# Performance work log

Hardware: AMD Instinct MI355X
Metric: run time of the kernel (lower is better)

The kernel has to match this reference:

```python
import jax, jax.numpy as jnp
import numpy as np

B, S, D = 4, 2048, 768
H, R = 12, 8
Dh = D // H


def setup_inputs() -> dict:
    key = jax.random.key(0)
    ks = jax.random.split(key, 12)
    s_in = 1.0 / np.sqrt(D)
    s_r = 1.0 / np.sqrt(R)
    return {
        "x": jax.random.normal(ks[0], (B, S, D), jnp.float32),
        "Wq0": jax.random.normal(ks[1], (D, D), jnp.float32) * s_in,
        "Aq": jax.random.normal(ks[2], (D, R), jnp.float32) * s_in,
        "Bq": jax.random.normal(ks[3], (R, D), jnp.float32) * s_r,
        "Wk0": jax.random.normal(ks[4], (D, D), jnp.float32) * s_in,
        "Ak": jax.random.normal(ks[5], (D, R), jnp.float32) * s_in,
        "Bk": jax.random.normal(ks[6], (R, D), jnp.float32) * s_r,
        "Wv0": jax.random.normal(ks[7], (D, D), jnp.float32) * s_in,
        "Av": jax.random.normal(ks[8], (D, R), jnp.float32) * s_in,
        "Bv": jax.random.normal(ks[9], (R, D), jnp.float32) * s_r,
        "Wo": jax.random.normal(ks[10], (D, D), jnp.float32) * s_in,
        "bo": jnp.zeros((D,), jnp.float32),
    }


def _lora(x, W0, A, Bm):
    # x @ W0 + (x @ A) @ B  -- low-rank adapter on frozen W0
    return x @ W0 + (x @ A) @ Bm


def _split_heads(t):
    # [B,S,D] -> [B,H,S,Dh]
    return t.reshape(B, S, H, Dh).transpose(0, 2, 1, 3)


def reference(x, Wq0, Aq, Bq, Wk0, Ak, Bk, Wv0, Av, Bv, Wo, bo):
    q = _split_heads(_lora(x, Wq0, Aq, Bq))
    k = _split_heads(_lora(x, Wk0, Ak, Bk))
    v = _split_heads(_lora(x, Wv0, Av, Bv))
    scale = 1.0 / jnp.sqrt(jnp.asarray(Dh, x.dtype))
    scores = jnp.einsum("bhqd,bhkd->bhqk", q, k) * scale  # [B,H,S,S]
    weights = jax.nn.softmax(scores, axis=-1)
    attn = jnp.einsum("bhqk,bhkd->bhqd", weights, v)
    concat = attn.transpose(0, 2, 1, 3).reshape(B, S, D)
    return concat @ Wo + bo
```

## Files before the change

kernel.cpp:

```cpp
#include <hip/hip_runtime.h>
#include <hip/hip_bf16.h>


typedef unsigned short ushort_t;
typedef __bf16 bf16x8 __attribute__((ext_vector_type(8)));
typedef float f32x4 __attribute__((ext_vector_type(4)));
typedef float f32x16 __attribute__((ext_vector_type(16)));
typedef unsigned short ushort8 __attribute__((ext_vector_type(8)));
typedef unsigned short ushort4_t __attribute__((ext_vector_type(4)));
typedef unsigned int uint4v __attribute__((ext_vector_type(4)));
typedef __attribute__((address_space(1))) unsigned int gu32;
typedef __attribute__((address_space(3))) unsigned int lu32;

__device__ __forceinline__ unsigned short f2bf(float f) {
  unsigned int u = __builtin_bit_cast(unsigned int, f);
  u += 0x7fffu + ((u >> 16) & 1u);
  return (unsigned short)(u >> 16);
}

__device__ __forceinline__ void gld_lds16(const void* g, void* s) {
  __builtin_amdgcn_global_load_lds((gu32*)(unsigned long long)g,
                                   (lu32*)(unsigned int)(unsigned long long)s,
                                   16, 0, 0);
}

__device__ __forceinline__ void gld_lds4(const void* g, void* s) {
  __builtin_amdgcn_global_load_lds((gu32*)(unsigned long long)g,
                                   (lu32*)(unsigned int)(unsigned long long)s,
                                   4, 0, 0);
}

__device__ __forceinline__ f32x4 mfma16(bf16x8 a, bf16x8 b, f32x4 c) {
  return __builtin_amdgcn_mfma_f32_16x16x32_bf16(a, b, c, 0, 0, 0);
}

__device__ __forceinline__ f32x16 mfma32(bf16x8 a, bf16x8 b, f32x16 c) {
  return __builtin_amdgcn_mfma_f32_32x32x16_bf16(a, b, c, 0, 0, 0);
}

__device__ __forceinline__ unsigned int cvtpk(float a, float b) {
  unsigned int r;
  asm("v_cvt_pk_bf16_f32 %0, %1, %2" : "=v"(r) : "v"(a), "v"(b));
  return r;
}

__global__ __launch_bounds__(256) void prep_weights(
    const float* __restrict__ Wq0, const float* __restrict__ Aq, const float* __restrict__ Bq,
    const float* __restrict__ Wk0, const float* __restrict__ Ak, const float* __restrict__ Bk,
    const float* __restrict__ Wv0, const float* __restrict__ Av, const float* __restrict__ Bv,
    const float* __restrict__ Wo,
    ushort_t* __restrict__ WeffT, ushort_t* __restrict__ WoT)
{
  __shared__ float tile[32][33];
  __shared__ float tA[32][8];
  __shared__ float tB[8][32];
  const int mat = blockIdx.y;
  const int kt = blockIdx.x / 24, nt = blockIdx.x % 24;
  const int k0 = kt * 32, n0 = nt * 32;
  const float* W0 = (mat == 0) ? Wq0 : (mat == 1) ? Wk0 : (mat == 2) ? Wv0 : Wo;
  const float* Am = (mat == 0) ? Aq : (mat == 1) ? Ak : (mat == 2) ? Av : nullptr;
  const float* Bm = (mat == 0) ? Bq : (mat == 1) ? Bk : (mat == 2) ? Bv : nullptr;
  const int tid = threadIdx.x;
#pragma unroll
  for (int i = 0; i < 4; i++) {
    int rr = i * 8 + (tid >> 5), c = tid & 31;
    tile[rr][c] = W0[(k0 + rr) * 768 + n0 + c];
  }
  if (Am) {
    tA[tid >> 3][tid & 7] = Am[(k0 + (tid >> 3)) * 8 + (tid & 7)];
    tB[tid >> 5][tid & 31] = Bm[(tid >> 5) * 768 + n0 + (tid & 31)];
  }
  __syncthreads();
#pragma unroll
  for (int i = 0; i < 4; i++) {
    int kk = tid & 31;
    int nn = i * 8 + (tid >> 5);
    float val = tile[kk][nn];
    if (Am) {
#pragma unroll
      for (int rr = 0; rr < 8; rr++) val += tA[kk][rr] * tB[rr][nn];
    }
    int n = n0 + nn, kg = k0 + kk;
    if (mat < 3) WeffT[((long)mat * 768 + n) * 768 + kg] = f2bf(val);
    else         WoT[(long)n * 768 + kg] = f2bf(val);
  }
}

__global__ __launch_bounds__(256) void cast_x(const float* __restrict__ x,
                                              ushort_t* __restrict__ xb)
{
  long i = (long)blockIdx.x * 256 + threadIdx.x;
  const float4* xp = (const float4*)x;
  float4 a = xp[i * 2], c = xp[i * 2 + 1];
  ushort8 rv;
  rv[0] = f2bf(a.x); rv[1] = f2bf(a.y); rv[2] = f2bf(a.z); rv[3] = f2bf(a.w);
  rv[4] = f2bf(c.x); rv[5] = f2bf(c.y); rv[6] = f2bf(c.z); rv[7] = f2bf(c.w);
  *(ushort8*)&xb[i * 8] = rv;
}

template <int MODE>
__global__ __launch_bounds__(256) void gemm_bt(
    const ushort_t* __restrict__ A, const ushort_t* __restrict__ Bt,
    ushort_t* __restrict__ q, ushort_t* __restrict__ kbuf, ushort_t* __restrict__ vt,
    float* __restrict__ out, const float* __restrict__ bo)
{
  constexpr int K = 768;
  __shared__ ushort_t As[128 * 64];
  __shared__ ushort_t Bs[128 * 64];
  const int tid = threadIdx.x;
  const int l = tid & 63, w = tid >> 6;
  const int wm = w >> 1, wn = w & 1;
  const int lr = l & 15, lg = l >> 4;
  const long rowBase = (long)blockIdx.x * 128;
  const long colBase = (long)blockIdx.y * 128;
  f32x4 acc[4][4] = {};

  for (int k0 = 0; k0 < K; k0 += 64) {
    __syncthreads();
#pragma unroll
    for (int i = 0; i < 4; i++) {
      int ci = i * 256 + tid;
      gld_lds16(A + (rowBase + (ci >> 3)) * K + k0 + (ci & 7) * 8, &As[ci * 8]);
    }
#pragma unroll
    for (int i = 0; i < 4; i++) {
      int ci = i * 256 + tid;
      gld_lds16(Bt + (colBase + (ci >> 3)) * K + k0 + (ci & 7) * 8, &Bs[ci * 8]);
    }
    asm volatile("s_waitcnt vmcnt(0)" ::: "memory");
    __syncthreads();
#pragma unroll
    for (int ks = 0; ks < 2; ks++) {
      bf16x8 af[4], bf[4];
#pragma unroll
      for (int m = 0; m < 4; m++)
        af[m] = *(const bf16x8*)&As[(wm * 64 + m * 16 + lr) * 64 + ks * 32 + lg * 8];
#pragma unroll
      for (int n = 0; n < 4; n++)
        bf[n] = *(const bf16x8*)&Bs[(wn * 64 + n * 16 + lr) * 64 + ks * 32 + lg * 8];
#pragma unroll
      for (int m = 0; m < 4; m++)
#pragma unroll
        for (int n = 0; n < 4; n++)
          acc[m][n] = mfma16(af[m], bf[n], acc[m][n]);
    }
  }

  if (MODE == 0) {
    const int mat = (int)(colBase / 768);
    if (mat == 2) {
      const long cb = colBase - 1536;
#pragma unroll
      for (int m = 0; m < 4; m++) {
        long srow = rowBase + wm * 64 + m * 16 + lg * 4;
        long b = srow >> 11, s = srow & 2047;
#pragma unroll
        for (int n = 0; n < 4; n++) {
          long col = cb + wn * 64 + n * 16 + lr;
          ushort4_t pk;
#pragma unroll
          for (int r = 0; r < 4; r++) pk[r] = f2bf(acc[m][n][r]);
          *(ushort4_t*)&vt[(b * 768 + col) * 2048 + s] = pk;
        }
      }
    } else {
      ushort_t* dst = (mat == 0) ? q : kbuf;
      const float scl = (mat == 0) ? 0.125f * 1.4426950408889634f : 1.0f;
      const long cb = colBase - (long)mat * 768;
#pragma unroll
      for (int m = 0; m < 4; m++)
#pragma unroll
        for (int n = 0; n < 4; n++) {
          long col = cb + wn * 64 + n * 16 + lr;
#pragma unroll
          for (int r = 0; r < 4; r++) {
            long row = rowBase + wm * 64 + m * 16 + lg * 4 + r;
            dst[row * 768 + col] = f2bf(acc[m][n][r] * scl);
          }
        }
    }
  } else {
#pragma unroll
    for (int m = 0; m < 4; m++)
#pragma unroll
      for (int n = 0; n < 4; n++) {
        long col = colBase + wn * 64 + n * 16 + lr;
        float bv = bo[col];
#pragma unroll
        for (int r = 0; r < 4; r++) {
          long row = rowBase + wm * 64 + m * 16 + lg * 4 + r;
          out[row * 768 + col] = acc[m][n][r] + bv;
        }
      }
  }
}

__global__ __launch_bounds__(256) void attn_fwd(
    const ushort_t* __restrict__ Q, const ushort_t* __restrict__ Kg,
    const ushort_t* __restrict__ VtG, ushort_t* __restrict__ O)
{
  constexpr int D = 768, S = 2048;
  __shared__ ushort_t Ks[2][64 * 64];
  __shared__ ushort_t Vs[2][64 * 64];
  const int tid = threadIdx.x;
  const int l = tid & 63, w = tid >> 6;
  const int q32 = l & 31, hi = l >> 5;
  const int i = blockIdx.x;
  const int xcd = i & 7, j = i >> 3;
  const int bh = xcd * 6 + (j >> 4);
  const int q0 = (j & 15) * 128;
  const int b = bh / 12, h = bh % 12;
  const ushort_t* Qb = Q + (long)b * S * D + h * 64;
  const ushort_t* Kb = Kg + (long)b * S * D + h * 64;
  const ushort_t* Vb = VtG + ((long)b * 768 + h * 64) * S;

  bf16x8 qf[4];
  {
    const ushort_t* qrow = Qb + (long)(q0 + w * 32 + q32) * D + hi * 8;
#pragma unroll
    for (int ks = 0; ks < 4; ks++) qf[ks] = *(const bf16x8*)&qrow[ks * 16];
  }

  int koff[2];
#pragma unroll
  for (int it = 0; it < 2; it++) {
    int ci = it * 256 + tid, r = ci >> 3, bp = ci & 7;
    koff[it] = r * D + ((bp ^ (r & 7)) * 8);
  }
  int voff[8];
#pragma unroll
  for (int it = 0; it < 8; it++) {
    int vi = it * 256 + tid;
    int d = vi >> 5, c_l = (vi >> 2) & 7, slot = vi & 3;
    int c = c_l ^ (d & 7);
    int p = c * 8 + slot * 2;
    int a = p >> 4, hp = (p >> 3) & 1, jj = p & 7;
    int key = 32 * (a >> 1) + 16 * (a & 1) + 8 * (jj >> 2) + (jj & 3) + 4 * hp;
    voff[it] = d * S + key;
  }

  bf16x8 ones;
#pragma unroll
  for (int e = 0; e < 8; e++) ones[e] = (__bf16)1.0f;

  f32x16 oA = {}, oB = {}, osum = {};
  const int swz = q32 & 7;

  auto STAGE = [&](int kt, int bi) {
    const ushort_t* kp = Kb + (long)kt * 64 * D;
#pragma unroll
    for (int it = 0; it < 2; it++)
      gld_lds16(kp + koff[it], &Ks[bi][(it * 256 + tid) * 8]);
    const ushort_t* vp = Vb + kt * 64;
#pragma unroll
    for (int it = 0; it < 8; it++)
      gld_lds4(vp + voff[it], &Vs[bi][(it * 256 + tid) * 2]);
  };

  STAGE(0, 0);

  for (int kt = 0; kt < 32; kt++) {
    const int cur = kt & 1;
    STAGE((kt + 1) & 31, cur ^ 1);
    asm volatile("s_waitcnt vmcnt(10)" ::: "memory");
    __builtin_amdgcn_s_barrier();

    const ushort_t* ksb = &Ks[cur][0];
    const ushort_t* vsb = &Vs[cur][0];

    f32x16 s0 = {}, s1 = {};
    __builtin_amdgcn_s_setprio(1);
#pragma unroll
    for (int ks = 0; ks < 4; ks++) {
      int ch = ((ks * 2 + hi) ^ swz) * 8;
      bf16x8 kf0 = *(const bf16x8*)&ksb[q32 * 64 + ch];
      bf16x8 kf1 = *(const bf16x8*)&ksb[(32 + q32) * 64 + ch];
      s0 = mfma32(kf0, qf[ks], s0);
      s1 = mfma32(kf1, qf[ks], s1);
    }
    __builtin_amdgcn_s_setprio(0);

    unsigned int pw[16];
#pragma unroll
    for (int u = 0; u < 8; u++) {
      float a0 = __builtin_amdgcn_exp2f(s0[2 * u]);
      float a1 = __builtin_amdgcn_exp2f(s0[2 * u + 1]);
      pw[u] = cvtpk(a0, a1);
    }
#pragma unroll
    for (int u = 0; u < 8; u++) {
      float a0 = __builtin_amdgcn_exp2f(s1[2 * u]);
      float a1 = __builtin_amdgcn_exp2f(s1[2 * u + 1]);
      pw[8 + u] = cvtpk(a0, a1);
    }

    __builtin_amdgcn_s_setprio(1);
#pragma unroll
    for (int ks = 0; ks < 4; ks++) {
      uint4v w4 = {pw[4 * ks], pw[4 * ks + 1], pw[4 * ks + 2], pw[4 * ks + 3]};
      bf16x8 pa = __builtin_bit_cast(bf16x8, w4);
      int ch = ((ks * 2 + hi) ^ swz) * 8;
      bf16x8 vf0 = *(const bf16x8*)&vsb[q32 * 64 + ch];
      bf16x8 vf1 = *(const bf16x8*)&vsb[(32 + q32) * 64 + ch];
      oA = mfma32(pa, vf0, oA);
      oB = mfma32(pa, vf1, oB);
      osum = mfma32(pa, ones, osum);
    }
    __builtin_amdgcn_s_setprio(0);

    asm volatile("" ::: "memory");
    __builtin_amdgcn_s_barrier();
  }

#pragma unroll
  for (int reg = 0; reg < 16; reg++) {
    int row = (reg & 3) + 8 * (reg >> 2) + 4 * hi;
    float inv = 1.0f / osum[reg];
    long base = ((long)b * S + q0 + w * 32 + row) * D + h * 64 + q32;
    O[base] = f2bf(oA[reg] * inv);
    O[base + 32] = f2bf(oB[reg] * inv);
  }
}

extern "C" void kernel_launch(void* const* d_in, const int* in_sizes, int n_in,
                              void* d_out, int out_size, void* d_ws, size_t ws_size,
                              hipStream_t stream)
{
  const float* x   = (const float*)d_in[0];
  const float* Wq0 = (const float*)d_in[1];
  const float* Aq  = (const float*)d_in[2];
  const float* Bq  = (const float*)d_in[3];
  const float* Wk0 = (const float*)d_in[4];
  const float* Ak  = (const float*)d_in[5];
  const float* Bk  = (const float*)d_in[6];
  const float* Wv0 = (const float*)d_in[7];
  const float* Av  = (const float*)d_in[8];
  const float* Bv  = (const float*)d_in[9];
  const float* Wo  = (const float*)d_in[10];
  const float* bo  = (const float*)d_in[11];
  float* out = (float*)d_out;

  char* ws = (char*)d_ws;
  const long SZ = 8192L * 768 * 2;
  ushort_t* xb    = (ushort_t*)(ws);
  ushort_t* Qb    = (ushort_t*)(ws + SZ);
  ushort_t* Kb    = (ushort_t*)(ws + 2 * SZ);
  ushort_t* Vt    = (ushort_t*)(ws + 3 * SZ);
  ushort_t* At    = (ushort_t*)(ws + 4 * SZ);
  ushort_t* WeffT = (ushort_t*)(ws + 5 * SZ);
  ushort_t* WoT   = (ushort_t*)(ws + 5 * SZ + 2304L * 768 * 2);

  hipLaunchKernelGGL(prep_weights, dim3(576, 4), dim3(256), 0, stream,
                     Wq0, Aq, Bq, Wk0, Ak, Bk, Wv0, Av, Bv, Wo, WeffT, WoT);
  hipLaunchKernelGGL(cast_x, dim3(3072), dim3(256), 0, stream, x, xb);
  hipLaunchKernelGGL((gemm_bt<0>), dim3(64, 18), dim3(256), 0, stream,
                     xb, WeffT, Qb, Kb, Vt, (float*)nullptr, (const float*)nullptr);
  hipLaunchKernelGGL(attn_fwd, dim3(768), dim3(256), 0, stream, Qb, Kb, Vt, At);
  hipLaunchKernelGGL((gemm_bt<1>), dim3(64, 6), dim3(256), 0, stream,
                     At, WoT, (ushort_t*)nullptr, (ushort_t*)nullptr, (ushort_t*)nullptr,
                     out, bo);
}
```

Measured before the change: 174.9 us.

## Pre-permute V^T key order in projection epilogue to enable 16-byte LDS loads

The V-projection epilogue now writes V^T with key positions permuted (bits 2 and 3 of the sequence index swapped), matching the order the P-fragment MFMA layout expects. The attention kernel can then stage V tiles with two 16-byte global-to-LDS loads per thread instead of eight 4-byte loads, using the same XOR swizzle as K. The wait count is lowered to match, and the per-ks read offsets are precomputed. This couples the producer layout to the consumer's register layout, so any mismatch would silently give wrong results.

```diff
diff --git a/kernel.cpp b/kernel.cpp
--- a/kernel.cpp
+++ b/kernel.cpp
@@ -22,12 +22,6 @@
   __builtin_amdgcn_global_load_lds((gu32*)(unsigned long long)g,
                                    (lu32*)(unsigned int)(unsigned long long)s,
                                    16, 0, 0);
-}
-
-__device__ __forceinline__ void gld_lds4(const void* g, void* s) {
-  __builtin_amdgcn_global_load_lds((gu32*)(unsigned long long)g,
-                                   (lu32*)(unsigned int)(unsigned long long)s,
-                                   4, 0, 0);
 }
 
 __device__ __forceinline__ f32x4 mfma16(bf16x8 a, bf16x8 b, f32x4 c) {
@@ -154,13 +148,14 @@
       for (int m = 0; m < 4; m++) {
         long srow = rowBase + wm * 64 + m * 16 + lg * 4;
         long b = srow >> 11, s = srow & 2047;
+        long sp = (s & ~12L) | ((s & 4) << 1) | ((s & 8) >> 1);
 #pragma unroll
         for (int n = 0; n < 4; n++) {
           long col = cb + wn * 64 + n * 16 + lr;
           ushort4_t pk;
 #pragma unroll
           for (int r = 0; r < 4; r++) pk[r] = f2bf(acc[m][n][r]);
-          *(ushort4_t*)&vt[(b * 768 + col) * 2048 + s] = pk;
+          *(ushort4_t*)&vt[(b * 768 + col) * 2048 + sp] = pk;
         }
       }
     } else {
@@ -221,40 +216,33 @@
     for (int ks = 0; ks < 4; ks++) qf[ks] = *(const bf16x8*)&qrow[ks * 16];
   }
 
-  int koff[2];
+  int koff[2], voff[2];
 #pragma unroll
   for (int it = 0; it < 2; it++) {
-    int ci = it * 256 + tid, r = ci >> 3, bp = ci & 7;
-    koff[it] = r * D + ((bp ^ (r & 7)) * 8);
-  }
-  int voff[8];
-#pragma unroll
-  for (int it = 0; it < 8; it++) {
-    int vi = it * 256 + tid;
-    int d = vi >> 5, c_l = (vi >> 2) & 7, slot = vi & 3;
-    int c = c_l ^ (d & 7);
-    int p = c * 8 + slot * 2;
-    int a = p >> 4, hp = (p >> 3) & 1, jj = p & 7;
-    int key = 32 * (a >> 1) + 16 * (a & 1) + 8 * (jj >> 2) + (jj & 3) + 4 * hp;
-    voff[it] = d * S + key;
-  }
+    int ci = it * 256 + tid, r = ci >> 3, c = ci & 7;
+    koff[it] = r * D + ((c ^ (r & 7)) * 8);
+    voff[it] = r * S + ((c ^ (r & 7)) * 8);
+  }
+  const int swz = q32 & 7;
+  int rdoff[4];
+#pragma unroll
+  for (int ks = 0; ks < 4; ks++) rdoff[ks] = ((ks * 2 + hi) ^ swz) * 8;
 
   bf16x8 ones;
 #pragma unroll
   for (int e = 0; e < 8; e++) ones[e] = (__bf16)1.0f;
 
   f32x16 oA = {}, oB = {}, osum = {};
-  const int swz = q32 & 7;
 
   auto STAGE = [&](int kt, int bi) {
     const ushort_t* kp = Kb + (long)kt * 64 * D;
+    const ushort_t* vp = Vb + kt * 64;
 #pragma unroll
     for (int it = 0; it < 2; it++)
       gld_lds16(kp + koff[it], &Ks[bi][(it * 256 + tid) * 8]);
-    const ushort_t* vp = Vb + kt * 64;
-#pragma unroll
-    for (int it = 0; it < 8; it++)
-      gld_lds4(vp + voff[it], &Vs[bi][(it * 256 + tid) * 2]);
+#pragma unroll
+    for (int it = 0; it < 2; it++)
+      gld_lds16(vp + voff[it], &Vs[bi][(it * 256 + tid) * 8]);
   };
 
   STAGE(0, 0);
@@ -262,7 +250,7 @@
   for (int kt = 0; kt < 32; kt++) {
     const int cur = kt & 1;
     STAGE((kt + 1) & 31, cur ^ 1);
-    asm volatile("s_waitcnt vmcnt(10)" ::: "memory");
+    asm volatile("s_waitcnt vmcnt(4)" ::: "memory");
     __builtin_amdgcn_s_barrier();
 
     const ushort_t* ksb = &Ks[cur][0];
@@ -272,9 +260,8 @@
     __builtin_amdgcn_s_setprio(1);
 #pragma unroll
     for (int ks = 0; ks < 4; ks++) {
-      int ch = ((ks * 2 + hi) ^ swz) * 8;
-      bf16x8 kf0 = *(const bf16x8*)&ksb[q32 * 64 + ch];
-      bf16x8 kf1 = *(const bf16x8*)&ksb[(32 + q32) * 64 + ch];
+      bf16x8 kf0 = *(const bf16x8*)&ksb[q32 * 64 + rdoff[ks]];
+      bf16x8 kf1 = *(const bf16x8*)&ksb[(32 + q32) * 64 + rdoff[ks]];
       s0 = mfma32(kf0, qf[ks], s0);
       s1 = mfma32(kf1, qf[ks], s1);
     }
@@ -299,9 +286,8 @@
     for (int ks = 0; ks < 4; ks++) {
       uint4v w4 = {pw[4 * ks], pw[4 * ks + 1], pw[4 * ks + 2], pw[4 * ks + 3]};
       bf16x8 pa = __builtin_bit_cast(bf16x8, w4);
-      int ch = ((ks * 2 + hi) ^ swz) * 8;
-      bf16x8 vf0 = *(const bf16x8*)&vsb[q32 * 64 + ch];
-      bf16x8 vf1 = *(const bf16x8*)&vsb[(32 + q32) * 64 + ch];
+      bf16x8 vf0 = *(const bf16x8*)&vsb[q32 * 64 + rdoff[ks]];
+      bf16x8 vf1 = *(const bf16x8*)&vsb[(32 + q32) * 64 + rdoff[ks]];
       oA = mfma32(pa, vf0, oA);
       oB = mfma32(pa, vf1, oB);
       osum = mfma32(pa, ones, osum);
```

Measured after the change: 174.8 us. About the same (-0.1%).
